# Performance work log

Hardware: AMD Instinct MI355X
Metric: run time of the kernel (lower is better)

## Reference

```python
import jax, jax.numpy as jnp
import numpy as np

B, N, E = 4, 10000, 170000
F_IN, F, H = 256, 128, 4
LEAKY_SLOPE = 0.2  # TF default alpha for tf.nn.leaky_relu


def setup_inputs() -> dict:
    key = jax.random.key(0)
    ks = jax.random.split(key, 6)
    x = jax.random.normal(ks[0], (B, N, F_IN), jnp.float32)
    src = jnp.sort(jax.random.randint(ks[1], (E,), 0, N, jnp.int32))
    dst = jax.random.randint(ks[2], (E,), 0, N, jnp.int32)
    W_mlp = jax.random.normal(ks[3], (H, F_IN, F), jnp.float32) / np.float32(np.sqrt(F_IN))
    b_mlp = jnp.zeros((H, F), jnp.float32)
    W_attn = jax.random.normal(ks[4], (H, 2 * F, 1), jnp.float32) / np.float32(np.sqrt(2 * F))
    return {"x": x, "W_mlp": W_mlp, "b_mlp": b_mlp, "W_attn": W_attn, "src": src, "dst": dst}


def reference(x, W_mlp, b_mlp, W_attn, src, dst):
    n_edges = src.shape[0]
    batch = x.shape[0]
    # per-head node transform: [B,H,N,F]
    h = jnp.einsum('bnf,hfe->bhne', x, W_mlp) + b_mlp[None, :, None, :]
    # split attention kernel: score = leaky_relu([h_src||h_dst] @ W_attn)
    a_src = W_attn[:, :F, 0]  # [H,F]
    a_dst = W_attn[:, F:, 0]  # [H,F]
    # faithful quirk: the original normalizes and scatters attention from the
    # LAST batch element only (attention_scores[-1]) and applies it to all batches
    hl = h[-1]  # [H,N,F]
    p_src = jnp.einsum('hnf,hf->hn', hl, a_src)
    p_dst = jnp.einsum('hnf,hf->hn', hl, a_dst)
    s = p_src[:, src] + p_dst[:, dst]                 # [H,E]
    e = jnp.exp(jnp.clip(jax.nn.leaky_relu(s, LEAKY_SLOPE), -2.0, 2.0))
    denom = jax.ops.segment_sum(e.T, src, num_segments=N).T  # [H,N]
    norm = e / denom[:, src]                          # [H,E]
    outs = []
    for hi in range(H):  # small fixed head loop (limits peak memory)
        g = jnp.take(h[:, hi], dst, axis=1) * norm[hi][None, :, None]  # [B,E,F]
        g = jnp.swapaxes(g, 0, 1).reshape(n_edges, batch * F)          # [E,B*F]
        agg = jax.ops.segment_sum(g, src, num_segments=N)              # [N,B*F]
        outs.append(agg.reshape(N, batch, F).transpose(1, 0, 2))       # [B,N,F]
    return jnp.concatenate(outs, axis=-1)  # [B,N,H*F]
```

## Files before the change

kernel.cpp:

```cpp
#include <hip/hip_runtime.h>
#include <hip/hip_bf16.h>

constexpr int Bq  = 4;
constexpr int Nn  = 10000;
constexpr int Eq  = 170000;
constexpr int FIN = 256;
constexpr int Ff  = 128;
constexpr int Hh  = 4;
constexpr int Mrows = Nn * Bq;
constexpr int C   = Hh * Ff;
constexpr float LEAKY = 0.2f;

typedef short short4v __attribute__((ext_vector_type(4)));
typedef short short8  __attribute__((ext_vector_type(8)));
typedef float f32x4   __attribute__((ext_vector_type(4)));

static __device__ __forceinline__ unsigned short f2bf(float f) {
    unsigned int u = __float_as_uint(f);
    u = u + 0x7fffu + ((u >> 16) & 1u);
    return (unsigned short)(u >> 16);
}
static __device__ __forceinline__ float bf2f(unsigned short b) {
    return __uint_as_float(((unsigned int)b) << 16);
}

__global__ __launch_bounds__(256) void xprep2_kernel(
    const float* __restrict__ X, unsigned short* __restrict__ Xb)
{
    int n0 = blockIdx.x * 8;
    int t  = threadIdx.x;
    int r  = t >> 5;
    int k8 = (t & 31) * 8;
    #pragma unroll
    for (int b = 0; b < Bq; ++b) {
        const float* p = X + ((size_t)b * Nn + n0 + r) * FIN + k8;
        float4 v0 = *(const float4*)p, v1 = *(const float4*)(p + 4);
        short8 v;
        v[0] = (short)f2bf(v0.x); v[1] = (short)f2bf(v0.y);
        v[2] = (short)f2bf(v0.z); v[3] = (short)f2bf(v0.w);
        v[4] = (short)f2bf(v1.x); v[5] = (short)f2bf(v1.y);
        v[6] = (short)f2bf(v1.z); v[7] = (short)f2bf(v1.w);
        *(short8*)(Xb + ((size_t)(n0 + r) * Bq + b) * FIN + k8) = v;
    }
}

__global__ void wprep_kernel(const float* __restrict__ W, unsigned short* __restrict__ Wf)
{
    int c = blockIdx.x;
    int k = threadIdx.x;
    float v = W[(size_t)(c >> 7) * FIN * Ff + (size_t)k * Ff + (c & 127)];
    int w = c >> 7, j = (c >> 4) & 7, ln = c & 15;
    int ks = k >> 5, quad = (k >> 3) & 3, el = k & 7;
    size_t u = ((size_t)((w * 8 + j) * 8 + ks) * 4 + quad) * 16 + ln;
    Wf[u * 8 + el] = f2bf(v);
}

__global__ __launch_bounds__(256) void waprep_kernel(
    const float* __restrict__ W, const float* __restrict__ Wattn,
    const float* __restrict__ bmlp, float* __restrict__ wa, float* __restrict__ bsd)
{
    int t = threadIdx.x;
    int hi = t >> 6, kb = t & 63;
    #pragma unroll
    for (int i = 0; i < 4; ++i) {
        int k = kb + i * 64;
        float ss = 0.f, sd = 0.f;
        const float* wrow = W + ((size_t)hi * FIN + k) * Ff;
        const float* as = Wattn + hi * 2 * Ff;
        const float* ad = as + Ff;
        for (int f = 0; f < Ff; f += 4) {
            float4 wv = *(const float4*)(wrow + f);
            float4 av = *(const float4*)(as + f);
            float4 dv = *(const float4*)(ad + f);
            ss += wv.x * av.x + wv.y * av.y + wv.z * av.z + wv.w * av.w;
            sd += wv.x * dv.x + wv.y * dv.y + wv.z * dv.z + wv.w * dv.w;
        }
        wa[(0 * 4 + hi) * FIN + k] = ss;
        wa[(1 * 4 + hi) * FIN + k] = sd;
    }
    if (t < 8) {
        int v = t & 1, hh = t >> 1;
        float s = 0.f;
        for (int f = 0; f < Ff; ++f)
            s += bmlp[hh * Ff + f] * Wattn[hh * 2 * Ff + v * Ff + f];
        bsd[v * 4 + hh] = s;
    }
}

__global__ __launch_bounds__(256) void pproj_kernel(
    const float* __restrict__ X, const float* __restrict__ wa,
    const float* __restrict__ bsd, float* __restrict__ psT, float* __restrict__ pdT)
{
    int wave = threadIdx.x >> 6, l = threadIdx.x & 63;
    int n = blockIdx.x * 4 + wave;
    if (n >= Nn) return;
    float4 xv = *(const float4*)(X + ((size_t)(Bq - 1) * Nn + n) * FIN + l * 4);
    float s[8];
    #pragma unroll
    for (int i = 0; i < 8; ++i) {
        float4 wv = *(const float4*)(wa + (size_t)i * FIN + l * 4);
        s[i] = xv.x * wv.x + xv.y * wv.y + xv.z * wv.z + xv.w * wv.w;
    }
    #pragma unroll
    for (int off = 1; off < 64; off <<= 1)
        #pragma unroll
        for (int i = 0; i < 8; ++i) s[i] += __shfl_xor(s[i], off, 64);
    if (l == 0) {
        #pragma unroll
        for (int hi = 0; hi < 4; ++hi) {
            psT[n * 4 + hi] = s[hi]     + bsd[hi];
            pdT[n * 4 + hi] = s[4 + hi] + bsd[4 + hi];
        }
    }
}

__global__ void row_start_kernel(const int* __restrict__ src, int* __restrict__ row_start)
{
    int n = blockIdx.x * blockDim.x + threadIdx.x;
    if (n > Nn) return;
    int lo = 0, hi = Eq;
    while (lo < hi) { int mid = (lo + hi) >> 1; if (src[mid] < n) lo = mid + 1; else hi = mid; }
    row_start[n] = lo;
}

__global__ __launch_bounds__(64) void edge_denom_kernel(
    const int* __restrict__ dst, const int* __restrict__ row_start,
    const float* __restrict__ psT, const float* __restrict__ pdT,
    float* __restrict__ eed, float* __restrict__ denom)
{
    int n = blockIdx.x, t = threadIdx.x;
    int e0 = row_start[n], e1 = row_start[n + 1];
    float4 ps = *(const float4*)(psT + (size_t)n * 4);
    float4 acc = {0.f, 0.f, 0.f, 0.f};
    for (int e = e0 + t; e < e1; e += 64) {
        int d = dst[e];
        float4 pd = *(const float4*)(pdT + (size_t)d * 4);
        float4 ev;
        {
            float sc = ps.x + pd.x; float lr = sc > 0.f ? sc : LEAKY * sc;
            ev.x = __expf(fminf(fmaxf(lr, -2.f), 2.f));
        }
        {
            float sc = ps.y + pd.y; float lr = sc > 0.f ? sc : LEAKY * sc;
            ev.y = __expf(fminf(fmaxf(lr, -2.f), 2.f));
        }
        {
            float sc = ps.z + pd.z; float lr = sc > 0.f ? sc : LEAKY * sc;
            ev.z = __expf(fminf(fmaxf(lr, -2.f), 2.f));
        }
        {
            float sc = ps.w + pd.w; float lr = sc > 0.f ? sc : LEAKY * sc;
            ev.w = __expf(fminf(fmaxf(lr, -2.f), 2.f));
        }
        *(float4*)(eed + (size_t)e * 4) = ev;
        acc.x += ev.x; acc.y += ev.y; acc.z += ev.z; acc.w += ev.w;
    }
    #pragma unroll
    for (int off = 32; off; off >>= 1) {
        acc.x += __shfl_down(acc.x, off, 64);
        acc.y += __shfl_down(acc.y, off, 64);
        acc.z += __shfl_down(acc.z, off, 64);
        acc.w += __shfl_down(acc.w, off, 64);
    }
    if (t == 0) *(float4*)(denom + (size_t)n * 4) = acc;
}

__global__ __launch_bounds__(256) void gather_kernel(
    const unsigned short* __restrict__ Xb, const float* __restrict__ eed,
    const float* __restrict__ denom, const int* __restrict__ row_start,
    const int* __restrict__ dst, unsigned short* __restrict__ Gx)
{
    int n = blockIdx.x, t = threadIdx.x;
    int e0 = row_start[n], e1 = row_start[n + 1];
    float4 dn = *(const float4*)(denom + (size_t)n * 4);
    float inv0 = dn.x != 0.f ? 1.f / dn.x : 0.f;
    float inv1 = dn.y != 0.f ? 1.f / dn.y : 0.f;
    float inv2 = dn.z != 0.f ? 1.f / dn.z : 0.f;
    float inv3 = dn.w != 0.f ? 1.f / dn.w : 0.f;

    float acc[4][4];
    #pragma unroll
    for (int hi = 0; hi < 4; ++hi)
        #pragma unroll
        for (int j = 0; j < 4; ++j) acc[hi][j] = 0.f;

    const float4* eed4 = (const float4*)eed;
    int off = t * 4;

    int e = e0;
    for (; e + 4 <= e1; e += 4) {
        int d0 = dst[e], d1 = dst[e + 1], d2 = dst[e + 2], d3 = dst[e + 3];
        short4v v0 = *(const short4v*)(Xb + (size_t)d0 * 1024 + off);
        short4v v1 = *(const short4v*)(Xb + (size_t)d1 * 1024 + off);
        short4v v2 = *(const short4v*)(Xb + (size_t)d2 * 1024 + off);
        short4v v3 = *(const short4v*)(Xb + (size_t)d3 * 1024 + off);
        float4 ev0 = eed4[e], ev1 = eed4[e + 1], ev2 = eed4[e + 2], ev3 = eed4[e + 3];
        float w[4][4] = {
            {ev0.x * inv0, ev0.y * inv1, ev0.z * inv2, ev0.w * inv3},
            {ev1.x * inv0, ev1.y * inv1, ev1.z * inv2, ev1.w * inv3},
            {ev2.x * inv0, ev2.y * inv1, ev2.z * inv2, ev2.w * inv3},
            {ev3.x * inv0, ev3.y * inv1, ev3.z * inv2, ev3.w * inv3}};
        #pragma unroll
        for (int j = 0; j < 4; ++j) {
            float f0 = bf2f((unsigned short)v0[j]);
            float f1 = bf2f((unsigned short)v1[j]);
            float f2 = bf2f((unsigned short)v2[j]);
            float f3 = bf2f((unsigned short)v3[j]);
            #pragma unroll
            for (int hi = 0; hi < 4; ++hi)
                acc[hi][j] += f0 * w[0][hi] + f1 * w[1][hi] + f2 * w[2][hi] + f3 * w[3][hi];
        }
    }
    for (; e < e1; ++e) {
        int d0 = dst[e];
        short4v v0 = *(const short4v*)(Xb + (size_t)d0 * 1024 + off);
        float4 ev0 = eed4[e];
        float w0 = ev0.x * inv0, w1 = ev0.y * inv1, w2 = ev0.z * inv2, w3 = ev0.w * inv3;
        #pragma unroll
        for (int j = 0; j < 4; ++j) {
            float f = bf2f((unsigned short)v0[j]);
            acc[0][j] += f * w0; acc[1][j] += f * w1;
            acc[2][j] += f * w2; acc[3][j] += f * w3;
        }
    }

    int b = t >> 6, k0 = (t & 63) * 4;
    #pragma unroll
    for (int hi = 0; hi < 4; ++hi) {
        short4v o;
        #pragma unroll
        for (int j = 0; j < 4; ++j) o[j] = (short)f2bf(acc[hi][j]);
        *(short4v*)(Gx + ((size_t)hi * Mrows + (size_t)n * 4 + b) * FIN + k0) = o;
    }
}

__global__ __launch_bounds__(256) void gemm2_kernel(
    const unsigned short* __restrict__ Gx, const unsigned short* __restrict__ Wf,
    const float* __restrict__ bias, const float* __restrict__ denom,
    float* __restrict__ out)
{
    __shared__ unsigned short As[32][264];

    const int hi = blockIdx.y;
    const int r0 = blockIdx.x * 32;
    const int tid = threadIdx.x;
    const int wave = tid >> 6, lane = tid & 63;
    const int quad = lane >> 4, ln = lane & 15;

    const unsigned short* Arows = Gx + ((size_t)hi * Mrows + r0) * FIN;
    #pragma unroll
    for (int i = 0; i < 4; ++i) {
        int u = tid + i * 256;
        int row = u >> 5, cu = u & 31;
        *(short8*)&As[row][cu * 8] = *(const short8*)(Arows + (size_t)row * FIN + cu * 8);
    }
    __syncthreads();

    f32x4 acc[2][2];
    #pragma unroll
    for (int i = 0; i < 2; ++i)
        #pragma unroll
        for (int j = 0; j < 2; ++j) acc[i][j] = (f32x4){0.f, 0.f, 0.f, 0.f};

    const short8* Wf8 = (const short8*)Wf;
    #pragma unroll
    for (int ks = 0; ks < 8; ++ks) {
        short8 a0 = *(const short8*)&As[ln][ks * 32 + quad * 8];
        short8 a1 = *(const short8*)&As[16 + ln][ks * 32 + quad * 8];
        #pragma unroll
        for (int jj = 0; jj < 2; ++jj) {
            int j = wave * 2 + jj;
            short8 b = Wf8[(size_t)((hi * 8 + j) * 8 + ks) * 64 + lane];
            acc[0][jj] = __builtin_amdgcn_mfma_f32_16x16x32_bf16(a0, b, acc[0][jj], 0, 0, 0);
            acc[1][jj] = __builtin_amdgcn_mfma_f32_16x16x32_bf16(a1, b, acc[1][jj], 0, 0, 0);
        }
    }

    #pragma unroll
    for (int jj = 0; jj < 2; ++jj) {
        int colf = (wave * 2 + jj) * 16 + ln;
        float bv = bias[hi * Ff + colf];
        #pragma unroll
        for (int mt = 0; mt < 2; ++mt) {
            #pragma unroll
            for (int r = 0; r < 4; ++r) {
                int m = mt * 16 + quad * 4 + r;
                int g = r0 + m;
                int nn = g >> 2, bb = g & 3;
                float flag = denom[(size_t)nn * 4 + hi] != 0.f ? 1.f : 0.f;
                out[((size_t)bb * Nn + nn) * C + hi * Ff + colf] = acc[mt][jj][r] + bv * flag;
            }
        }
    }
}

extern "C" void kernel_launch(void* const* d_in, const int* in_sizes, int n_in,
                              void* d_out, int out_size, void* d_ws, size_t ws_size,
                              hipStream_t stream)
{
    const float* x      = (const float*)d_in[0];
    const float* W_mlp  = (const float*)d_in[1];
    const float* b_mlp  = (const float*)d_in[2];
    const float* W_attn = (const float*)d_in[3];
    const int*   src    = (const int*)d_in[4];
    const int*   dst    = (const int*)d_in[5];
    float* out = (float*)d_out;

    unsigned short* Gx  = (unsigned short*)d_ws;
    unsigned short* Xb  = Gx + (size_t)Hh * Mrows * FIN;
    unsigned short* Wf  = Xb + (size_t)Nn * Bq * FIN;
    float* eed   = (float*)(Wf + (size_t)C * FIN);
    float* psT   = eed + (size_t)Eq * 4;
    float* pdT   = psT + (size_t)Nn * 4;
    float* denom = pdT + (size_t)Nn * 4;
    float* wa    = denom + (size_t)Nn * 4;
    float* bsd   = wa + 2 * 4 * FIN;
    int*   row_st = (int*)(bsd + 16);

    hipLaunchKernelGGL(xprep2_kernel, dim3(Nn / 8), dim3(256), 0, stream, x, Xb);
    hipLaunchKernelGGL(wprep_kernel, dim3(C), dim3(FIN), 0, stream, W_mlp, Wf);
    hipLaunchKernelGGL(waprep_kernel, dim3(1), dim3(256), 0, stream,
                       W_mlp, W_attn, b_mlp, wa, bsd);
    hipLaunchKernelGGL(pproj_kernel, dim3(Nn / 4), dim3(256), 0, stream,
                       x, wa, bsd, psT, pdT);
    hipLaunchKernelGGL(row_start_kernel, dim3((Nn + 256) / 256), dim3(256), 0, stream,
                       src, row_st);
    hipLaunchKernelGGL(edge_denom_kernel, dim3(Nn), dim3(64), 0, stream,
                       dst, row_st, psT, pdT, eed, denom);
    hipLaunchKernelGGL(gather_kernel, dim3(Nn), dim3(256), 0, stream,
                       Xb, eed, denom, row_st, dst, Gx);
    hipLaunchKernelGGL(gemm2_kernel, dim3(Mrows / 32, Hh), dim3(256), 0, stream,
                       Gx, Wf, b_mlp, denom, out);
}
```

Before: 239.3 us.

## Fuse gather with GEMM via shared memory and fuse x-prep with attention projection

The per-node edge gather now writes its aggregated bf16 rows into shared memory, and the same block immediately runs the MFMA projection for all four heads. This removes the Gx round trip through global memory and one kernel launch. The x-to-bf16 conversion also computes the attention projections for the last batch, which drops the separate pproj pass over x, and edge_denom now packs four nodes per 256-thread block. In exchange the fused kernel has only 1250 blocks that each loop over 8 nodes serially, so occupancy and parallelism drop, and the larger shared tile and accumulator set may raise register pressure.

```diff
diff --git a/kernel.cpp b/kernel.cpp
--- a/kernel.cpp
+++ b/kernel.cpp
@@ -7,7 +7,6 @@
 constexpr int FIN = 256;
 constexpr int Ff  = 128;
 constexpr int Hh  = 4;
-constexpr int Mrows = Nn * Bq;
 constexpr int C   = Hh * Ff;
 constexpr float LEAKY = 0.2f;
 
@@ -24,13 +23,20 @@
     return __uint_as_float(((unsigned int)b) << 16);
 }
 
-__global__ __launch_bounds__(256) void xprep2_kernel(
-    const float* __restrict__ X, unsigned short* __restrict__ Xb)
+__global__ __launch_bounds__(256) void xprep_proj_kernel(
+    const float* __restrict__ X, const float* __restrict__ wa,
+    const float* __restrict__ bsd, unsigned short* __restrict__ Xb,
+    float* __restrict__ psT, float* __restrict__ pdT)
 {
     int n0 = blockIdx.x * 8;
     int t  = threadIdx.x;
     int r  = t >> 5;
-    int k8 = (t & 31) * 8;
+    int c  = t & 31;
+    int k8 = c * 8;
+    float s[8];
+    #pragma unroll
+    for (int i = 0; i < 8; ++i) s[i] = 0.f;
+
     #pragma unroll
     for (int b = 0; b < Bq; ++b) {
         const float* p = X + ((size_t)b * Nn + n0 + r) * FIN + k8;
@@ -41,15 +47,36 @@
         v[4] = (short)f2bf(v1.x); v[5] = (short)f2bf(v1.y);
         v[6] = (short)f2bf(v1.z); v[7] = (short)f2bf(v1.w);
         *(short8*)(Xb + ((size_t)(n0 + r) * Bq + b) * FIN + k8) = v;
+        if (b == Bq - 1) {
+            #pragma unroll
+            for (int i = 0; i < 8; ++i) {
+                const float* w = wa + (size_t)i * FIN + k8;
+                float4 w0 = *(const float4*)w, w1 = *(const float4*)(w + 4);
+                s[i] = v0.x * w0.x + v0.y * w0.y + v0.z * w0.z + v0.w * w0.w
+                     + v1.x * w1.x + v1.y * w1.y + v1.z * w1.z + v1.w * w1.w;
+            }
+        }
+    }
+    #pragma unroll
+    for (int off = 1; off < 32; off <<= 1)
+        #pragma unroll
+        for (int i = 0; i < 8; ++i) s[i] += __shfl_xor(s[i], off, 64);
+    if (c == 0) {
+        int n = n0 + r;
+        #pragma unroll
+        for (int hi = 0; hi < 4; ++hi) {
+            psT[n * 4 + hi] = s[hi]     + bsd[hi];
+            pdT[n * 4 + hi] = s[4 + hi] + bsd[4 + hi];
+        }
     }
 }
 
 __global__ void wprep_kernel(const float* __restrict__ W, unsigned short* __restrict__ Wf)
 {
-    int c = blockIdx.x;
+    int cc = blockIdx.x;
     int k = threadIdx.x;
-    float v = W[(size_t)(c >> 7) * FIN * Ff + (size_t)k * Ff + (c & 127)];
-    int w = c >> 7, j = (c >> 4) & 7, ln = c & 15;
+    float v = W[(size_t)(cc >> 7) * FIN * Ff + (size_t)k * Ff + (cc & 127)];
+    int w = cc >> 7, j = (cc >> 4) & 7, ln = cc & 15;
     int ks = k >> 5, quad = (k >> 3) & 3, el = k & 7;
     size_t u = ((size_t)((w * 8 + j) * 8 + ks) * 4 + quad) * 16 + ln;
     Wf[u * 8 + el] = f2bf(v);
@@ -87,33 +114,6 @@
     }
 }
 
-__global__ __launch_bounds__(256) void pproj_kernel(
-    const float* __restrict__ X, const float* __restrict__ wa,
-    const float* __restrict__ bsd, float* __restrict__ psT, float* __restrict__ pdT)
-{
-    int wave = threadIdx.x >> 6, l = threadIdx.x & 63;
-    int n = blockIdx.x * 4 + wave;
-    if (n >= Nn) return;
-    float4 xv = *(const float4*)(X + ((size_t)(Bq - 1) * Nn + n) * FIN + l * 4);
-    float s[8];
-    #pragma unroll
-    for (int i = 0; i < 8; ++i) {
-        float4 wv = *(const float4*)(wa + (size_t)i * FIN + l * 4);
-        s[i] = xv.x * wv.x + xv.y * wv.y + xv.z * wv.z + xv.w * wv.w;
-    }
-    #pragma unroll
-    for (int off = 1; off < 64; off <<= 1)
-        #pragma unroll
-        for (int i = 0; i < 8; ++i) s[i] += __shfl_xor(s[i], off, 64);
-    if (l == 0) {
-        #pragma unroll
-        for (int hi = 0; hi < 4; ++hi) {
-            psT[n * 4 + hi] = s[hi]     + bsd[hi];
-            pdT[n * 4 + hi] = s[4 + hi] + bsd[4 + hi];
-        }
-    }
-}
-
 __global__ void row_start_kernel(const int* __restrict__ src, int* __restrict__ row_start)
 {
     int n = blockIdx.x * blockDim.x + threadIdx.x;
@@ -123,12 +123,13 @@
     row_start[n] = lo;
 }
 
-__global__ __launch_bounds__(64) void edge_denom_kernel(
+__global__ __launch_bounds__(256) void edge_denom_kernel(
     const int* __restrict__ dst, const int* __restrict__ row_start,
     const float* __restrict__ psT, const float* __restrict__ pdT,
     float* __restrict__ eed, float* __restrict__ denom)
 {
-    int n = blockIdx.x, t = threadIdx.x;
+    int wv = threadIdx.x >> 6, t = threadIdx.x & 63;
+    int n = blockIdx.x * 4 + wv;
     int e0 = row_start[n], e1 = row_start[n + 1];
     float4 ps = *(const float4*)(psT + (size_t)n * 4);
     float4 acc = {0.f, 0.f, 0.f, 0.f};
@@ -136,22 +137,14 @@
         int d = dst[e];
         float4 pd = *(const float4*)(pdT + (size_t)d * 4);
         float4 ev;
-        {
-            float sc = ps.x + pd.x; float lr = sc > 0.f ? sc : LEAKY * sc;
-            ev.x = __expf(fminf(fmaxf(lr, -2.f), 2.f));
-        }
-        {
-            float sc = ps.y + pd.y; float lr = sc > 0.f ? sc : LEAKY * sc;
-            ev.y = __expf(fminf(fmaxf(lr, -2.f), 2.f));
-        }
-        {
-            float sc = ps.z + pd.z; float lr = sc > 0.f ? sc : LEAKY * sc;
-            ev.z = __expf(fminf(fmaxf(lr, -2.f), 2.f));
-        }
-        {
-            float sc = ps.w + pd.w; float lr = sc > 0.f ? sc : LEAKY * sc;
-            ev.w = __expf(fminf(fmaxf(lr, -2.f), 2.f));
-        }
+        { float sc = ps.x + pd.x; float lr = sc > 0.f ? sc : LEAKY * sc;
+          ev.x = __expf(fminf(fmaxf(lr, -2.f), 2.f)); }
+        { float sc = ps.y + pd.y; float lr = sc > 0.f ? sc : LEAKY * sc;
+          ev.y = __expf(fminf(fmaxf(lr, -2.f), 2.f)); }
+        { float sc = ps.z + pd.z; float lr = sc > 0.f ? sc : LEAKY * sc;
+          ev.z = __expf(fminf(fmaxf(lr, -2.f), 2.f)); }
+        { float sc = ps.w + pd.w; float lr = sc > 0.f ? sc : LEAKY * sc;
+          ev.w = __expf(fminf(fmaxf(lr, -2.f), 2.f)); }
         *(float4*)(eed + (size_t)e * 4) = ev;
         acc.x += ev.x; acc.y += ev.y; acc.z += ev.z; acc.w += ev.w;
     }
@@ -165,130 +158,119 @@
     if (t == 0) *(float4*)(denom + (size_t)n * 4) = acc;
 }
 
-__global__ __launch_bounds__(256) void gather_kernel(
+__global__ __launch_bounds__(256) void gather_gemm_kernel(
     const unsigned short* __restrict__ Xb, const float* __restrict__ eed,
     const float* __restrict__ denom, const int* __restrict__ row_start,
-    const int* __restrict__ dst, unsigned short* __restrict__ Gx)
-{
-    int n = blockIdx.x, t = threadIdx.x;
-    int e0 = row_start[n], e1 = row_start[n + 1];
-    float4 dn = *(const float4*)(denom + (size_t)n * 4);
-    float inv0 = dn.x != 0.f ? 1.f / dn.x : 0.f;
-    float inv1 = dn.y != 0.f ? 1.f / dn.y : 0.f;
-    float inv2 = dn.z != 0.f ? 1.f / dn.z : 0.f;
-    float inv3 = dn.w != 0.f ? 1.f / dn.w : 0.f;
-
-    float acc[4][4];
-    #pragma unroll
-    for (int hi = 0; hi < 4; ++hi)
-        #pragma unroll
-        for (int j = 0; j < 4; ++j) acc[hi][j] = 0.f;
-
+    const int* __restrict__ dst, const unsigned short* __restrict__ Wf,
+    const float* __restrict__ bias, float* __restrict__ out)
+{
+    __shared__ unsigned short gx[4][32][264];
+
+    const int n0 = blockIdx.x * 8;
+    const int t  = threadIdx.x;
+    const int b  = t >> 6;
+    const int k0 = (t & 63) * 4;
     const float4* eed4 = (const float4*)eed;
-    int off = t * 4;
-
-    int e = e0;
-    for (; e + 4 <= e1; e += 4) {
-        int d0 = dst[e], d1 = dst[e + 1], d2 = dst[e + 2], d3 = dst[e + 3];
-        short4v v0 = *(const short4v*)(Xb + (size_t)d0 * 1024 + off);
-        short4v v1 = *(const short4v*)(Xb + (size_t)d1 * 1024 + off);
-        short4v v2 = *(const short4v*)(Xb + (size_t)d2 * 1024 + off);
-        short4v v3 = *(const short4v*)(Xb + (size_t)d3 * 1024 + off);
-        float4 ev0 = eed4[e], ev1 = eed4[e + 1], ev2 = eed4[e + 2], ev3 = eed4[e + 3];
-        float w[4][4] = {
-            {ev0.x * inv0, ev0.y * inv1, ev0.z * inv2, ev0.w * inv3},
-            {ev1.x * inv0, ev1.y * inv1, ev1.z * inv2, ev1.w * inv3},
-            {ev2.x * inv0, ev2.y * inv1, ev2.z * inv2, ev2.w * inv3},
-            {ev3.x * inv0, ev3.y * inv1, ev3.z * inv2, ev3.w * inv3}};
-        #pragma unroll
-        for (int j = 0; j < 4; ++j) {
-            float f0 = bf2f((unsigned short)v0[j]);
-            float f1 = bf2f((unsigned short)v1[j]);
-            float f2 = bf2f((unsigned short)v2[j]);
-            float f3 = bf2f((unsigned short)v3[j]);
-            #pragma unroll
-            for (int hi = 0; hi < 4; ++hi)
-                acc[hi][j] += f0 * w[0][hi] + f1 * w[1][hi] + f2 * w[2][hi] + f3 * w[3][hi];
-        }
-    }
-    for (; e < e1; ++e) {
-        int d0 = dst[e];
-        short4v v0 = *(const short4v*)(Xb + (size_t)d0 * 1024 + off);
-        float4 ev0 = eed4[e];
-        float w0 = ev0.x * inv0, w1 = ev0.y * inv1, w2 = ev0.z * inv2, w3 = ev0.w * inv3;
-        #pragma unroll
-        for (int j = 0; j < 4; ++j) {
-            float f = bf2f((unsigned short)v0[j]);
-            acc[0][j] += f * w0; acc[1][j] += f * w1;
-            acc[2][j] += f * w2; acc[3][j] += f * w3;
-        }
-    }
-
-    int b = t >> 6, k0 = (t & 63) * 4;
-    #pragma unroll
-    for (int hi = 0; hi < 4; ++hi) {
-        short4v o;
-        #pragma unroll
-        for (int j = 0; j < 4; ++j) o[j] = (short)f2bf(acc[hi][j]);
-        *(short4v*)(Gx + ((size_t)hi * Mrows + (size_t)n * 4 + b) * FIN + k0) = o;
-    }
-}
-
-__global__ __launch_bounds__(256) void gemm2_kernel(
-    const unsigned short* __restrict__ Gx, const unsigned short* __restrict__ Wf,
-    const float* __restrict__ bias, const float* __restrict__ denom,
-    float* __restrict__ out)
-{
-    __shared__ unsigned short As[32][264];
-
-    const int hi = blockIdx.y;
-    const int r0 = blockIdx.x * 32;
-    const int tid = threadIdx.x;
-    const int wave = tid >> 6, lane = tid & 63;
+
+    for (int ni = 0; ni < 8; ++ni) {
+        int n = n0 + ni;
+        int e0 = row_start[n], e1 = row_start[n + 1];
+        float4 dn = *(const float4*)(denom + (size_t)n * 4);
+        float inv0 = dn.x != 0.f ? 1.f / dn.x : 0.f;
+        float inv1 = dn.y != 0.f ? 1.f / dn.y : 0.f;
+        float inv2 = dn.z != 0.f ? 1.f / dn.z : 0.f;
+        float inv3 = dn.w != 0.f ? 1.f / dn.w : 0.f;
+
+        float acc[4][4];
+        #pragma unroll
+        for (int hi = 0; hi < 4; ++hi)
+            #pragma unroll
+            for (int j = 0; j < 4; ++j) acc[hi][j] = 0.f;
+
+        size_t boff = (size_t)b * FIN + k0;
+        int e = e0;
+        for (; e + 4 <= e1; e += 4) {
+            int d0 = dst[e], d1 = dst[e + 1], d2 = dst[e + 2], d3 = dst[e + 3];
+            short4v v0 = *(const short4v*)(Xb + (size_t)d0 * 1024 + boff);
+            short4v v1 = *(const short4v*)(Xb + (size_t)d1 * 1024 + boff);
+            short4v v2 = *(const short4v*)(Xb + (size_t)d2 * 1024 + boff);
+            short4v v3 = *(const short4v*)(Xb + (size_t)d3 * 1024 + boff);
+            float4 ev0 = eed4[e], ev1 = eed4[e + 1], ev2 = eed4[e + 2], ev3 = eed4[e + 3];
+            float w[4][4] = {
+                {ev0.x * inv0, ev0.y * inv1, ev0.z * inv2, ev0.w * inv3},
+                {ev1.x * inv0, ev1.y * inv1, ev1.z * inv2, ev1.w * inv3},
+                {ev2.x * inv0, ev2.y * inv1, ev2.z * inv2, ev2.w * inv3},
+                {ev3.x * inv0, ev3.y * inv1, ev3.z * inv2, ev3.w * inv3}};
+            #pragma unroll
+            for (int j = 0; j < 4; ++j) {
+                float f0 = bf2f((unsigned short)v0[j]);
+                float f1 = bf2f((unsigned short)v1[j]);
+                float f2 = bf2f((unsigned short)v2[j]);
+                float f3 = bf2f((unsigned short)v3[j]);
+                #pragma unroll
+                for (int hi = 0; hi < 4; ++hi)
+                    acc[hi][j] += f0 * w[0][hi] + f1 * w[1][hi] + f2 * w[2][hi] + f3 * w[3][hi];
+            }
+        }
+        for (; e < e1; ++e) {
+            int d0 = dst[e];
+            short4v v0 = *(const short4v*)(Xb + (size_t)d0 * 1024 + boff);
+            float4 ev0 = eed4[e];
+            float w0 = ev0.x * inv0, w1 = ev0.y * inv1, w2 = ev0.z * inv2, w3 = ev0.w * inv3;
+            #pragma unroll
+            for (int j = 0; j < 4; ++j) {
+                float f = bf2f((unsigned short)v0[j]);
+                acc[0][j] += f * w0; acc[1][j] += f * w1;
+                acc[2][j] += f * w2; acc[3][j] += f * w3;
+            }
+        }
+
+        int row = ni * 4 + b;
+        #pragma unroll
+        for (int hi = 0; hi < 4; ++hi) {
+            short4v o;
+            #pragma unroll
+            for (int j = 0; j < 4; ++j) o[j] = (short)f2bf(acc[hi][j]);
+            *(short4v*)&gx[hi][row][k0] = o;
+        }
+    }
+    __syncthreads();
+
+    const int wave = t >> 6, lane = t & 63;
     const int quad = lane >> 4, ln = lane & 15;
-
-    const unsigned short* Arows = Gx + ((size_t)hi * Mrows + r0) * FIN;
-    #pragma unroll
-    for (int i = 0; i < 4; ++i) {
-        int u = tid + i * 256;
-        int row = u >> 5, cu = u & 31;
-        *(short8*)&As[row][cu * 8] = *(const short8*)(Arows + (size_t)row * FIN + cu * 8);
-    }
-    __syncthreads();
-
-    f32x4 acc[2][2];
+    const int hi = wave;
+
+    f32x4 macc[2][8];
     #pragma unroll
     for (int i = 0; i < 2; ++i)
         #pragma unroll
-        for (int j = 0; j < 2; ++j) acc[i][j] = (f32x4){0.f, 0.f, 0.f, 0.f};
+        for (int j = 0; j < 8; ++j) macc[i][j] = (f32x4){0.f, 0.f, 0.f, 0.f};
 
     const short8* Wf8 = (const short8*)Wf;
     #pragma unroll
     for (int ks = 0; ks < 8; ++ks) {
-        short8 a0 = *(const short8*)&As[ln][ks * 32 + quad * 8];
-        short8 a1 = *(const short8*)&As[16 + ln][ks * 32 + quad * 8];
-        #pragma unroll
-        for (int jj = 0; jj < 2; ++jj) {
-            int j = wave * 2 + jj;
-            short8 b = Wf8[(size_t)((hi * 8 + j) * 8 + ks) * 64 + lane];
-            acc[0][jj] = __builtin_amdgcn_mfma_f32_16x16x32_bf16(a0, b, acc[0][jj], 0, 0, 0);
-            acc[1][jj] = __builtin_amdgcn_mfma_f32_16x16x32_bf16(a1, b, acc[1][jj], 0, 0, 0);
-        }
-    }
-
-    #pragma unroll
-    for (int jj = 0; jj < 2; ++jj) {
-        int colf = (wave * 2 + jj) * 16 + ln;
+        short8 a0 = *(const short8*)&gx[hi][ln][ks * 32 + quad * 8];
+        short8 a1 = *(const short8*)&gx[hi][16 + ln][ks * 32 + quad * 8];
+        #pragma unroll
+        for (int j = 0; j < 8; ++j) {
+            short8 bf = Wf8[(size_t)((hi * 8 + j) * 8 + ks) * 64 + lane];
+            macc[0][j] = __builtin_amdgcn_mfma_f32_16x16x32_bf16(a0, bf, macc[0][j], 0, 0, 0);
+            macc[1][j] = __builtin_amdgcn_mfma_f32_16x16x32_bf16(a1, bf, macc[1][j], 0, 0, 0);
+        }
+    }
+
+    #pragma unroll
+    for (int j = 0; j < 8; ++j) {
+        int colf = j * 16 + ln;
         float bv = bias[hi * Ff + colf];
         #pragma unroll
         for (int mt = 0; mt < 2; ++mt) {
             #pragma unroll
             for (int r = 0; r < 4; ++r) {
                 int m = mt * 16 + quad * 4 + r;
-                int g = r0 + m;
-                int nn = g >> 2, bb = g & 3;
+                int nn = n0 + (m >> 2), bb = m & 3;
                 float flag = denom[(size_t)nn * 4 + hi] != 0.f ? 1.f : 0.f;
-                out[((size_t)bb * Nn + nn) * C + hi * Ff + colf] = acc[mt][jj][r] + bv * flag;
+                out[((size_t)bb * Nn + nn) * C + hi * Ff + colf] = macc[mt][j][r] + bv * flag;
             }
         }
     }
@@ -306,8 +288,7 @@
     const int*   dst    = (const int*)d_in[5];
     float* out = (float*)d_out;
 
-    unsigned short* Gx  = (unsigned short*)d_ws;
-    unsigned short* Xb  = Gx + (size_t)Hh * Mrows * FIN;
+    unsigned short* Xb  = (unsigned short*)d_ws;
     unsigned short* Wf  = Xb + (size_t)Nn * Bq * FIN;
     float* eed   = (float*)(Wf + (size_t)C * FIN);
     float* psT   = eed + (size_t)Eq * 4;
@@ -317,18 +298,15 @@
     float* bsd   = wa + 2 * 4 * FIN;
     int*   row_st = (int*)(bsd + 16);
 
-    hipLaunchKernelGGL(xprep2_kernel, dim3(Nn / 8), dim3(256), 0, stream, x, Xb);
     hipLaunchKernelGGL(wprep_kernel, dim3(C), dim3(FIN), 0, stream, W_mlp, Wf);
     hipLaunchKernelGGL(waprep_kernel, dim3(1), dim3(256), 0, stream,
                        W_mlp, W_attn, b_mlp, wa, bsd);
-    hipLaunchKernelGGL(pproj_kernel, dim3(Nn / 4), dim3(256), 0, stream,
-                       x, wa, bsd, psT, pdT);
     hipLaunchKernelGGL(row_start_kernel, dim3((Nn + 256) / 256), dim3(256), 0, stream,
                        src, row_st);
-    hipLaunchKernelGGL(edge_denom_kernel, dim3(Nn), dim3(64), 0, stream,
+    hipLaunchKernelGGL(xprep_proj_kernel, dim3(Nn / 8), dim3(256), 0, stream,
+                       x, wa, bsd, Xb, psT, pdT);
+    hipLaunchKernelGGL(edge_denom_kernel, dim3(Nn / 4), dim3(256), 0, stream,
                        dst, row_st, psT, pdT, eed, denom);
-    hipLaunchKernelGGL(gather_kernel, dim3(Nn), dim3(256), 0, stream,
-                       Xb, eed, denom, row_st, dst, Gx);
-    hipLaunchKernelGGL(gemm2_kernel, dim3(Mrows / 32, Hh), dim3(256), 0, stream,
-                       Gx, Wf, b_mlp, denom, out);
-}
+    hipLaunchKernelGGL(gather_gemm_kernel, dim3(Nn / 8), dim3(256), 0, stream,
+                       Xb, eed, denom, row_st, dst, Wf, b_mlp, out);
+}
```

After: 300.7 us. 1.26x slower.
